# Optimization experiments

Measured on AMD Instinct MI355X. Metric: run time of the kernel, lower is better.

Reference implementation:

```python
import jax, jax.numpy as jnp
import numpy as np
from jax import lax

G, NPER, K = 64, 1024, 512          # graphs, nodes per graph, kept per graph (ceil(0.5*1024))
N, E = G * NPER, 1_048_576          # total nodes, total edges
F, H, C = 128, 128, 10              # in_feats, hidden_dim, num_classes


def gcn(x, src, dst, ew, W, b, num_nodes):
    """PyG GCNConv: D^{-1/2}(A+I)D^{-1/2} X W + b, with edge weights ew."""
    xw = x @ W                                              # [N, H]
    deg = jax.ops.segment_sum(ew, dst, num_segments=num_nodes) + 1.0  # +1 self loop
    dinv = lax.rsqrt(deg)
    coef = dinv[src] * dinv[dst] * ew                       # [E]
    agg = jax.ops.segment_sum(coef[:, None] * xw[src], dst, num_segments=num_nodes)
    return agg + (dinv * dinv)[:, None] * xw + b            # self-loop term + bias


def setup_inputs() -> dict:
    key = jax.random.key(0)
    ks = jax.random.split(key, 10)
    x = jax.random.normal(ks[0], (N, F), jnp.float32)
    # intra-graph random edges: dst forced into same graph block as src
    src = jax.random.randint(ks[1], (E,), 0, N, dtype=jnp.int32)
    dst = (src // NPER) * NPER + jax.random.randint(ks[2], (E,), 0, NPER, dtype=jnp.int32)
    edge_index = jnp.stack([src, dst])                      # [2, E]
    batch = jnp.repeat(jnp.arange(G, dtype=jnp.int32), NPER)
    W1 = jax.random.normal(ks[3], (F, H), jnp.float32) / np.sqrt(F)
    b1 = jnp.zeros((H,), jnp.float32)
    p = jax.random.normal(ks[4], (H,), jnp.float32) / np.sqrt(H)   # TopKPooling score vector
    W2 = jax.random.normal(ks[5], (H, H), jnp.float32) / np.sqrt(H)
    b2 = jnp.zeros((H,), jnp.float32)
    Wl = jax.random.normal(ks[6], (H, C), jnp.float32) / np.sqrt(H)
    bl = jnp.zeros((C,), jnp.float32)
    return dict(x=x, edge_index=edge_index, batch=batch, W1=W1, b1=b1, p=p, W2=W2, b2=b2, Wl=Wl, bl=bl)


def reference(x, edge_index, batch, W1, b1, p, W2, b2, Wl, bl):
    src, dst = edge_index[0], edge_index[1]
    ew1 = jnp.ones((E,), x.dtype)
    h = jax.nn.relu(gcn(x, src, dst, ew1, W1, b1, N))       # conv1 + relu

    # --- TopKPooling: score = tanh(x.p/||p||), keep top-K per graph, gate x by score ---
    score = jnp.tanh((h @ p) / jnp.linalg.norm(p))          # [N]
    vals, idx = lax.top_k(score.reshape(G, NPER), K)        # per-graph top-k, [G, K]
    perm = (idx + jnp.arange(G, dtype=idx.dtype)[:, None] * NPER).reshape(-1)  # global ids [G*K]
    h2 = h[perm] * vals.reshape(-1, 1)                      # gated kept nodes [G*K, H]

    # edge re-index: keep only edges with both endpoints surviving (mask via weight 0)
    new_id = jnp.full((N,), -1, jnp.int32).at[perm].set(jnp.arange(G * K, dtype=jnp.int32))
    s2, d2 = new_id[src], new_id[dst]
    mask = (s2 >= 0) & (d2 >= 0)
    ew2 = mask.astype(h.dtype)
    s2 = jnp.where(mask, s2, 0)
    d2 = jnp.where(mask, d2, 0)

    h3 = jax.nn.relu(gcn(h2, s2, d2, ew2, W2, b2, G * K))   # conv2 + relu

    pooled = h3.reshape(G, K, H).mean(axis=1)               # global_mean_pool (equal counts)
    return pooled @ Wl + bl                                 # [G, C]
```

## Files before the change

### kernel.cpp

```cpp
#include <hip/hip_runtime.h>

#define NNODES 65536
#define NEDGES 1048576
#define NGRAPH 64
#define NPERG  1024
#define KEEP   512
#define M2     (NGRAPH * KEEP)
#define HD     128
#define NC     10
#define EMAX   20480

#define OW1 0
#define OW2 16384
#define OWL 32768
#define OB1 34048
#define OB2 34176
#define OP  34304
#define OBL 34432
#define NCVT 34448

typedef __attribute__((ext_vector_type(8))) short bf16x8;
typedef __attribute__((ext_vector_type(4))) float f32x4;

__device__ __forceinline__ float bf2f(unsigned short u) {
    return __uint_as_float(((unsigned int)u) << 16);
}
__device__ __forceinline__ unsigned short f2bf(float f) {
    unsigned int u = __float_as_uint(f);
    unsigned int r = (u + 0x7FFFu + ((u >> 16) & 1u)) >> 16;
    return (unsigned short)r;
}

__global__ __launch_bounds__(256) void prep_kernel(
    const void* __restrict__ W1, const void* __restrict__ b1, const void* __restrict__ p,
    const void* __restrict__ W2, const void* __restrict__ b2, const void* __restrict__ Wl,
    const void* __restrict__ bl, int* __restrict__ flag, float* __restrict__ cw,
    float* __restrict__ invnorm, int* __restrict__ new_id, int* __restrict__ ghist,
    int* __restrict__ gcur0, float* __restrict__ pooled,
    unsigned short* __restrict__ w1t, unsigned short* __restrict__ w2t,
    const int* __restrict__ src, int* __restrict__ phist) {
    int bid = blockIdx.x, t = threadIdx.x;
    const unsigned short* w1u = (const unsigned short*)W1;
    int local = 0;
    for (int i = t; i < 512; i += 256) {
        unsigned short u = w1u[2 * i];
        int e = (u >> 7) & 0xFF;
        local += (e >= 100 && e <= 140) ? 1 : 0;
    }
    __shared__ int red[256];
    __shared__ int lh[NGRAPH];
    red[t] = local;
    __syncthreads();
    for (int off = 128; off; off >>= 1) {
        if (t < off) red[t] += red[t + off];
        __syncthreads();
    }
    int fl = (red[0] >= 384) ? 1 : 0;
    if (bid == 0 && t == 0) flag[0] = fl;

    if (bid < 135) {
        int gid = bid * 256 + t;
        if (gid < NCVT) {
            const void* srcp; int idx;
            if (gid < OB1) {
                if (gid < OW2)      { srcp = W1; idx = gid - OW1; }
                else if (gid < OWL) { srcp = W2; idx = gid - OW2; }
                else                { srcp = Wl; idx = gid - OWL; }
            } else {
                if (gid < OB2)      { srcp = b1; idx = gid - OB1; }
                else if (gid < OP)  { srcp = b2; idx = gid - OB2; }
                else if (gid < OBL) { srcp = p;  idx = gid - OP; }
                else                { srcp = bl; idx = gid - OBL; }
            }
            float v;
            if (gid >= OWL && gid < OB1 && idx >= 1280) v = 0.f;
            else if (gid >= OBL && idx >= NC) v = 0.f;
            else if (fl) v = bf2f(((const unsigned short*)srcp)[idx]);
            else v = ((const float*)srcp)[idx];
            cw[gid] = v;
            if (gid < OW2) {
                int k = gid >> 7, n = gid & 127;
                w1t[n * 128 + k] = f2bf(v);
            } else if (gid < OWL) {
                int r = gid - OW2;
                int k = r >> 7, n = r & 127;
                w2t[n * 128 + k] = f2bf(v);
            }
        }
    } else if (bid == 135) {
        __shared__ float s2a[128];
        float pv = 0.f;
        if (t < 128) pv = fl ? bf2f(((const unsigned short*)p)[t]) : ((const float*)p)[t];
        if (t < 128) s2a[t] = pv * pv;
        __syncthreads();
        for (int off = 64; off; off >>= 1) {
            if (t < off) s2a[t] += s2a[t + off];
            __syncthreads();
        }
        if (t == 0) invnorm[0] = 1.0f / sqrtf(s2a[0]);
    } else if (bid < 392) {
        int i = (bid - 136) * 256 + t;
        new_id[i] = -1;
        if (i < NGRAPH) { ghist[i] = 0; gcur0[i] = 0; }
        if (i < NGRAPH * HD) pooled[i] = 0.f;
    } else {
        if (t < NGRAPH) lh[t] = 0;
        __syncthreads();
        int e0 = (bid - 392) * 4096;
        for (int k = 0; k < 16; k++) atomicAdd(&lh[src[e0 + k * 256 + t] >> 10], 1);
        __syncthreads();
        if (t < NGRAPH) phist[(bid - 392) * 64 + t] = lh[t];
    }
}

__global__ __launch_bounds__(256) void binpass_kernel(const int* __restrict__ src,
                                                      const int* __restrict__ dst,
                                                      const int* __restrict__ phist,
                                                      int* __restrict__ ghist,
                                                      int* __restrict__ gcur0,
                                                      unsigned int* __restrict__ elist) {
    __shared__ int gh[NGRAPH];
    __shared__ int gbS[NGRAPH];
    __shared__ int lh[NGRAPH];
    __shared__ int lbase[NGRAPH];
    __shared__ int qsum[4][NGRAPH];
    int tid = threadIdx.x;
    {
        int g = tid & 63, q = tid >> 6;
        int s = 0;
        for (int b = q * 64; b < q * 64 + 64; b++) s += phist[b * 64 + g];
        qsum[q][g] = s;
    }
    __syncthreads();
    if (tid < NGRAPH) {
        gh[tid] = qsum[0][tid] + qsum[1][tid] + qsum[2][tid] + qsum[3][tid];
        lh[tid] = 0;
        if (blockIdx.x == 0) ghist[tid] = gh[tid];
    }
    __syncthreads();
    if (tid == 0) {
        int s = 0;
        for (int i = 0; i < NGRAPH; i++) { gbS[i] = s; s += gh[i]; }
    }
    __syncthreads();
    int e0 = blockIdx.x * 4096;
    int gs[16]; unsigned int pk[16];
    for (int k = 0; k < 16; k++) {
        int e = e0 + k * 256 + tid;
        int s = src[e], d = dst[e];
        gs[k] = s >> 10;
        pk[k] = (unsigned)(s & 1023) | ((unsigned)(d & 1023) << 10);
        atomicAdd(&lh[gs[k]], 1);
    }
    __syncthreads();
    if (tid < NGRAPH) { lbase[tid] = gbS[tid] + atomicAdd(&gcur0[tid], lh[tid]); lh[tid] = 0; }
    __syncthreads();
    for (int k = 0; k < 16; k++) {
        int g = gs[k];
        int pos = lbase[g] + atomicAdd(&lh[g], 1);
        elist[pos] = pk[k];
    }
}

__global__ __launch_bounds__(1024) void g1csr_kernel(
    const unsigned int* __restrict__ elist, const int* __restrict__ ghist,
    unsigned short* __restrict__ csr16, int* __restrict__ node_base,
    int* __restrict__ deg_out, float* __restrict__ dinv_out,
    const void* __restrict__ Araw, const unsigned short* __restrict__ Wtb,
    unsigned int* __restrict__ Cb, const int* __restrict__ flag) {
    __shared__ unsigned short sc[EMAX];
    __shared__ int cnt[NPERG];
    __shared__ int cur[NPERG];
    __shared__ int wsum[16];
    __shared__ int gh[NGRAPH];
    __shared__ int baseS, nS;
    int bid = blockIdx.x, t = threadIdx.x;
    if (bid < NGRAPH) {
        int g = bid;
        cnt[t] = 0;
        if (t < NGRAPH) gh[t] = ghist[t];
        __syncthreads();
        if (t == 0) {
            int s = 0;
            for (int i = 0; i < g; i++) s += gh[i];
            baseS = s; nS = gh[g];
        }
        __syncthreads();
        int base = baseS;
        int n = nS; if (n > EMAX) n = EMAX;
        for (int j = t; j < n; j += 1024) atomicAdd(&cnt[(elist[base + j] >> 10) & 1023], 1);
        __syncthreads();
        int v = cnt[t];
        int lane = t & 63;
        int x = v;
        for (int off = 1; off < 64; off <<= 1) {
            int y = __shfl_up(x, off);
            if (lane >= off) x += y;
        }
        if (lane == 63) wsum[t >> 6] = x;
        __syncthreads();
        if (t < 16) {
            int wv = wsum[t];
            int wx = wv;
            for (int off = 1; off < 16; off <<= 1) {
                int y = __shfl_up(wx, off);
                if (t >= off) wx += y;
            }
            wsum[t] = wx - wv;
        }
        __syncthreads();
        int excl = x - v + wsum[t >> 6];
        cur[t] = excl;
        deg_out[g * NPERG + t] = v;
        dinv_out[g * NPERG + t] = rsqrtf((float)v + 1.0f);
        node_base[g * NPERG + t] = base + excl;
        __syncthreads();
        for (int j = t; j < n; j += 1024) {
            unsigned int pk = elist[base + j];
            int d = (pk >> 10) & 1023;
            int pos = atomicAdd(&cur[d], 1);
            sc[pos] = (unsigned short)(pk & 1023);
        }
        __syncthreads();
        for (int j = t; j < n; j += 1024) csr16[base + j] = sc[j];
        return;
    }
    int row0 = (bid - NGRAPH) * 256;
    int wave = t >> 6, lane = t & 63;
    int r0 = row0 + wave * 16;
    int row = r0 + (lane & 15);
    int ko = (lane >> 4) * 8;
    f32x4 acc[8];
#pragma unroll
    for (int c = 0; c < 8; c++) acc[c] = (f32x4){0.f, 0.f, 0.f, 0.f};
    bf16x8 afr[4];
    if (flag[0]) {
        const unsigned short* arow = (const unsigned short*)Araw + (size_t)row * HD + ko;
#pragma unroll
        for (int kk = 0; kk < 4; kk++) afr[kk] = *(const bf16x8*)(arow + kk * 32);
    } else {
        const float* arow = (const float*)Araw + (size_t)row * HD + ko;
#pragma unroll
        for (int kk = 0; kk < 4; kk++) {
            float4 f0 = *(const float4*)(arow + kk * 32);
            float4 f1 = *(const float4*)(arow + kk * 32 + 4);
            bf16x8 a;
            a[0] = (short)f2bf(f0.x); a[1] = (short)f2bf(f0.y);
            a[2] = (short)f2bf(f0.z); a[3] = (short)f2bf(f0.w);
            a[4] = (short)f2bf(f1.x); a[5] = (short)f2bf(f1.y);
            a[6] = (short)f2bf(f1.z); a[7] = (short)f2bf(f1.w);
            afr[kk] = a;
        }
    }
    const unsigned short* brow = Wtb + (lane & 15) * HD + ko;
#pragma unroll
    for (int kk = 0; kk < 4; kk++) {
#pragma unroll
        for (int c = 0; c < 8; c++) {
            bf16x8 b = *(const bf16x8*)(brow + c * 16 * HD + kk * 32);
            acc[c] = __builtin_amdgcn_mfma_f32_16x16x32_bf16(afr[kk], b, acc[c], 0, 0, 0);
        }
    }
    int orow0 = r0 + (lane >> 4) * 4;
    bool even = !(lane & 1);
#pragma unroll
    for (int c = 0; c < 8; c++) {
#pragma unroll
        for (int j = 0; j < 4; j++) {
            float v = acc[c][j];
            float pt = __shfl_xor(v, 1);
            if (even) {
                unsigned int u = (unsigned int)f2bf(v) | ((unsigned int)f2bf(pt) << 16);
                Cb[(size_t)(orow0 + j) * 64 + ((c * 16 + (lane & 15)) >> 1)] = u;
            }
        }
    }
}

__global__ __launch_bounds__(256) void s1_pull(const unsigned short* __restrict__ csr16,
                                               const int* __restrict__ node_base,
                                               const int* __restrict__ deg,
                                               const float* __restrict__ dinv,
                                               const unsigned int* __restrict__ xwb,
                                               const float* __restrict__ b1,
                                               const float* __restrict__ pvec,
                                               const float* __restrict__ invnorm,
                                               unsigned int* __restrict__ hb,
                                               float* __restrict__ score) {
    int b = blockIdx.x;
    int xcd = b & 7, j = b >> 3;
    int g = (j >> 8) * 8 + xcd;
    int n = g * NPERG + (j & 255) * 4 + (threadIdx.x >> 6);
    int lane = threadIdx.x & 63;
    int gb = g * NPERG;
    int base = node_base[n], cnt = deg[n];
    int e = 0; float ds = 0.f;
    if (lane < cnt) {
        e = csr16[base + lane];
        ds = dinv[gb + e];
    }
    float a0 = 0.f, a1 = 0.f;
    int klim = cnt < 64 ? cnt : 64;
    int k = 0;
    for (; k + 7 < klim; k += 8) {
        int s0 = __shfl(e, k),     s1 = __shfl(e, k + 1);
        int s2 = __shfl(e, k + 2), s3 = __shfl(e, k + 3);
        int s4 = __shfl(e, k + 4), s5 = __shfl(e, k + 5);
        int s6 = __shfl(e, k + 6), s7 = __shfl(e, k + 7);
        float d0 = __shfl(ds, k),     d1 = __shfl(ds, k + 1);
        float d2 = __shfl(ds, k + 2), d3 = __shfl(ds, k + 3);
        float d4 = __shfl(ds, k + 4), d5 = __shfl(ds, k + 5);
        float d6 = __shfl(ds, k + 6), d7 = __shfl(ds, k + 7);
        unsigned int u0 = xwb[(size_t)(gb + s0) * 64 + lane];
        unsigned int u1 = xwb[(size_t)(gb + s1) * 64 + lane];
        unsigned int u2 = xwb[(size_t)(gb + s2) * 64 + lane];
        unsigned int u3 = xwb[(size_t)(gb + s3) * 64 + lane];
        unsigned int u4 = xwb[(size_t)(gb + s4) * 64 + lane];
        unsigned int u5 = xwb[(size_t)(gb + s5) * 64 + lane];
        unsigned int u6 = xwb[(size_t)(gb + s6) * 64 + lane];
        unsigned int u7 = xwb[(size_t)(gb + s7) * 64 + lane];
        a0 += d0 * __uint_as_float(u0 << 16); a1 += d0 * __uint_as_float(u0 & 0xFFFF0000u);
        a0 += d1 * __uint_as_float(u1 << 16); a1 += d1 * __uint_as_float(u1 & 0xFFFF0000u);
        a0 += d2 * __uint_as_float(u2 << 16); a1 += d2 * __uint_as_float(u2 & 0xFFFF0000u);
        a0 += d3 * __uint_as_float(u3 << 16); a1 += d3 * __uint_as_float(u3 & 0xFFFF0000u);
        a0 += d4 * __uint_as_float(u4 << 16); a1 += d4 * __uint_as_float(u4 & 0xFFFF0000u);
        a0 += d5 * __uint_as_float(u5 << 16); a1 += d5 * __uint_as_float(u5 & 0xFFFF0000u);
        a0 += d6 * __uint_as_float(u6 << 16); a1 += d6 * __uint_as_float(u6 & 0xFFFF0000u);
        a0 += d7 * __uint_as_float(u7 << 16); a1 += d7 * __uint_as_float(u7 & 0xFFFF0000u);
    }
    for (; k + 3 < klim; k += 4) {
        int s0 = __shfl(e, k), s1 = __shfl(e, k + 1);
        int s2 = __shfl(e, k + 2), s3 = __shfl(e, k + 3);
        float d0 = __shfl(ds, k), d1 = __shfl(ds, k + 1);
        float d2 = __shfl(ds, k + 2), d3 = __shfl(ds, k + 3);
        unsigned int u0 = xwb[(size_t)(gb + s0) * 64 + lane];
        unsigned int u1 = xwb[(size_t)(gb + s1) * 64 + lane];
        unsigned int u2 = xwb[(size_t)(gb + s2) * 64 + lane];
        unsigned int u3 = xwb[(size_t)(gb + s3) * 64 + lane];
        a0 += d0 * __uint_as_float(u0 << 16); a1 += d0 * __uint_as_float(u0 & 0xFFFF0000u);
        a0 += d1 * __uint_as_float(u1 << 16); a1 += d1 * __uint_as_float(u1 & 0xFFFF0000u);
        a0 += d2 * __uint_as_float(u2 << 16); a1 += d2 * __uint_as_float(u2 & 0xFFFF0000u);
        a0 += d3 * __uint_as_float(u3 << 16); a1 += d3 * __uint_as_float(u3 & 0xFFFF0000u);
    }
    for (; k < klim; k++) {
        int sk = __shfl(e, k);
        float dk = __shfl(ds, k);
        unsigned int u = xwb[(size_t)(gb + sk) * 64 + lane];
        a0 += dk * __uint_as_float(u << 16); a1 += dk * __uint_as_float(u & 0xFFFF0000u);
    }
    for (; k < cnt; k++) {
        int sk = csr16[base + k];
        float dk = dinv[gb + sk];
        unsigned int u = xwb[(size_t)(gb + sk) * 64 + lane];
        a0 += dk * __uint_as_float(u << 16); a1 += dk * __uint_as_float(u & 0xFFFF0000u);
    }
    float dn = dinv[n];
    float self = dn * dn;
    unsigned int us = xwb[(size_t)n * 64 + lane];
    float2 bb = ((const float2*)b1)[lane];
    float h0 = fmaxf(dn * a0 + self * __uint_as_float(us << 16) + bb.x, 0.f);
    float h1 = fmaxf(dn * a1 + self * __uint_as_float(us & 0xFFFF0000u) + bb.y, 0.f);
    hb[(size_t)n * 64 + lane] = (unsigned int)f2bf(h0) | ((unsigned int)f2bf(h1) << 16);
    float2 pp = ((const float2*)pvec)[lane];
    float sv = h0 * pp.x + h1 * pp.y;
    for (int off = 32; off; off >>= 1) sv += __shfl_down(sv, off);
    if (lane == 0) score[n] = tanhf(sv * invnorm[0]);
}

__global__ __launch_bounds__(1024) void topk_kernel(const float* __restrict__ score,
                                                    float* __restrict__ vals,
                                                    int* __restrict__ perm,
                                                    int* __restrict__ new_id) {
    __shared__ float sv[1024];
    __shared__ int si[1024];
    int g = blockIdx.x, t = threadIdx.x;
    float v = score[g * NPERG + t];
    int idx = t;
    for (int k = 2; k <= 1024; k <<= 1) {
        for (int j = k >> 1; j > 0; j >>= 1) {
            bool desc = ((t & k) == 0);
            bool up = (t & j) != 0;
            float vb; int ib;
            if (j >= 64) {
                sv[t] = v; si[t] = idx;
                __syncthreads();
                vb = sv[t ^ j]; ib = si[t ^ j];
                bool cmp = (v > vb) || (v == vb && idx < ib);
                bool keep = up ? (cmp != desc) : (cmp == desc);
                if (!keep) { v = vb; idx = ib; }
                __syncthreads();
            } else {
                vb = __shfl_xor(v, j);
                ib = __shfl_xor(idx, j);
                bool cmp = (v > vb) || (v == vb && idx < ib);
                bool keep = up ? (cmp != desc) : (cmp == desc);
                if (!keep) { v = vb; idx = ib; }
            }
        }
    }
    if (t < KEEP) {
        int node = g * NPERG + idx;
        int slot = g * KEEP + t;
        vals[slot] = v;
        perm[slot] = node;
        new_id[node] = slot;
    }
}

__global__ __launch_bounds__(512) void g2deg_kernel(
    const unsigned int* __restrict__ elist, const int* __restrict__ ghist,
    const int* __restrict__ new_id, float* __restrict__ dinv2,
    const unsigned int* __restrict__ hb, const int* __restrict__ perm,
    const float* __restrict__ vals, const unsigned short* __restrict__ Wtb,
    unsigned int* __restrict__ Cb) {
    __shared__ int d2[KEEP];
    __shared__ int gh[NGRAPH];
    __shared__ int baseS, nS;
    int bid = blockIdx.x, t = threadIdx.x;
    if (bid < NGRAPH) {
        int g = bid;
        if (t < KEEP) d2[t] = 0;
        if (t < NGRAPH) gh[t] = ghist[t];
        __syncthreads();
        if (t == 0) {
            int s = 0;
            for (int i = 0; i < g; i++) s += gh[i];
            baseS = s; nS = gh[g];
        }
        __syncthreads();
        int base = baseS, n = nS;
        int gb = g * NPERG;
        int kb = g * KEEP;
        for (int j = t; j < n; j += 512) {
            unsigned int pk = elist[base + j];
            int s = pk & 1023, d = (pk >> 10) & 1023;
            int ns = new_id[gb + s], nd = new_id[gb + d];
            if (ns >= 0 && nd >= 0) atomicAdd(&d2[nd - kb], 1);
        }
        __syncthreads();
        if (t < KEEP) dinv2[kb + t] = rsqrtf((float)d2[t] + 1.0f);
        return;
    }
    int row0 = (bid - NGRAPH) * 128;
    int wave = t >> 6, lane = t & 63;
    int r0 = row0 + wave * 16;
    int m = r0 + (lane & 15);
    int ko = (lane >> 4) * 8;
    float sc = vals[m];
    const unsigned int* arow = hb + (size_t)perm[m] * 64 + (ko >> 1);
    bf16x8 afr[4];
#pragma unroll
    for (int kk = 0; kk < 4; kk++) {
        uint4 q = *(const uint4*)(arow + kk * 16);
        bf16x8 a;
        a[0] = (short)f2bf(bf2f((unsigned short)q.x) * sc);
        a[1] = (short)f2bf(bf2f((unsigned short)(q.x >> 16)) * sc);
        a[2] = (short)f2bf(bf2f((unsigned short)q.y) * sc);
        a[3] = (short)f2bf(bf2f((unsigned short)(q.y >> 16)) * sc);
        a[4] = (short)f2bf(bf2f((unsigned short)q.z) * sc);
        a[5] = (short)f2bf(bf2f((unsigned short)(q.z >> 16)) * sc);
        a[6] = (short)f2bf(bf2f((unsigned short)q.w) * sc);
        a[7] = (short)f2bf(bf2f((unsigned short)(q.w >> 16)) * sc);
        afr[kk] = a;
    }
    f32x4 acc[8];
#pragma unroll
    for (int c = 0; c < 8; c++) acc[c] = (f32x4){0.f, 0.f, 0.f, 0.f};
    const unsigned short* brow = Wtb + (lane & 15) * HD + ko;
#pragma unroll
    for (int kk = 0; kk < 4; kk++) {
#pragma unroll
        for (int c = 0; c < 8; c++) {
            bf16x8 b = *(const bf16x8*)(brow + c * 16 * HD + kk * 32);
            acc[c] = __builtin_amdgcn_mfma_f32_16x16x32_bf16(afr[kk], b, acc[c], 0, 0, 0);
        }
    }
    int orow0 = r0 + (lane >> 4) * 4;
    bool even = !(lane & 1);
#pragma unroll
    for (int c = 0; c < 8; c++) {
#pragma unroll
        for (int j = 0; j < 4; j++) {
            float v = acc[c][j];
            float pt = __shfl_xor(v, 1);
            if (even) {
                unsigned int u = (unsigned int)f2bf(v) | ((unsigned int)f2bf(pt) << 16);
                Cb[(size_t)(orow0 + j) * 64 + ((c * 16 + (lane & 15)) >> 1)] = u;
            }
        }
    }
}

__global__ __launch_bounds__(256) void s2_pull(const unsigned short* __restrict__ csr16,
                                               const int* __restrict__ node_base,
                                               const int* __restrict__ deg,
                                               const int* __restrict__ perm,
                                               const int* __restrict__ new_id,
                                               const float* __restrict__ dinv2,
                                               const unsigned int* __restrict__ xwb2,
                                               const float* __restrict__ b2,
                                               float* __restrict__ pooled) {
    __shared__ float pr[HD];
    __shared__ int cnk[4][64];
    __shared__ float cds[4][64];
    int tid = threadIdx.x;
    if (tid < HD) pr[tid] = 0.f;
    __syncthreads();
    int b = blockIdx.x;
    int xcd = b & 7, j = b >> 3;
    int g = (j >> 7) * 8 + xcd;
    int wv = tid >> 6;
    int m = g * KEEP + (j & 127) * 4 + wv;
    int lane = tid & 63;
    int node = perm[m];
    int gb = node & ~(NPERG - 1);
    int base = node_base[node], cnt = deg[node];
    int nk = 0; float ds = 0.f;
    if (lane < cnt) {
        int ns = new_id[gb + csr16[base + lane]];
        if (ns >= 0) { nk = ns; ds = dinv2[ns]; }
    }
    unsigned long long msk = __ballot(ds != 0.f);
    int pos = __popcll(msk & ((1ull << lane) - 1ull));
    if (ds != 0.f) { cnk[wv][pos] = nk; cds[wv][pos] = ds; }
    int na = __popcll(msk);
    float a0 = 0.f, a1 = 0.f;
    int k = 0;
    for (; k + 3 < na; k += 4) {
        int s0 = cnk[wv][k], s1 = cnk[wv][k + 1];
        int s2 = cnk[wv][k + 2], s3 = cnk[wv][k + 3];
        float d0 = cds[wv][k], d1 = cds[wv][k + 1];
        float d2 = cds[wv][k + 2], d3 = cds[wv][k + 3];
        unsigned int u0 = xwb2[(size_t)s0 * 64 + lane];
        unsigned int u1 = xwb2[(size_t)s1 * 64 + lane];
        unsigned int u2 = xwb2[(size_t)s2 * 64 + lane];
        unsigned int u3 = xwb2[(size_t)s3 * 64 + lane];
        a0 += d0 * __uint_as_float(u0 << 16); a1 += d0 * __uint_as_float(u0 & 0xFFFF0000u);
        a0 += d1 * __uint_as_float(u1 << 16); a1 += d1 * __uint_as_float(u1 & 0xFFFF0000u);
        a0 += d2 * __uint_as_float(u2 << 16); a1 += d2 * __uint_as_float(u2 & 0xFFFF0000u);
        a0 += d3 * __uint_as_float(u3 << 16); a1 += d3 * __uint_as_float(u3 & 0xFFFF0000u);
    }
    for (; k < na; k++) {
        int sk = cnk[wv][k];
        float dk = cds[wv][k];
        unsigned int u = xwb2[(size_t)sk * 64 + lane];
        a0 += dk * __uint_as_float(u << 16); a1 += dk * __uint_as_float(u & 0xFFFF0000u);
    }
    for (int kk = 64; kk < cnt; kk++) {
        int ns = new_id[gb + csr16[base + kk]];
        if (ns >= 0) {
            float dk = dinv2[ns];
            unsigned int u = xwb2[(size_t)ns * 64 + lane];
            a0 += dk * __uint_as_float(u << 16); a1 += dk * __uint_as_float(u & 0xFFFF0000u);
        }
    }
    float dn = dinv2[m];
    float self = dn * dn;
    unsigned int us = xwb2[(size_t)m * 64 + lane];
    float2 bb = ((const float2*)b2)[lane];
    float o0 = fmaxf(dn * a0 + self * __uint_as_float(us << 16) + bb.x, 0.f);
    float o1 = fmaxf(dn * a1 + self * __uint_as_float(us & 0xFFFF0000u) + bb.y, 0.f);
    atomicAdd(&pr[lane * 2], o0);
    atomicAdd(&pr[lane * 2 + 1], o1);
    __syncthreads();
    if (tid < HD) atomicAdd(&pooled[g * HD + tid], pr[tid]);
}

__global__ __launch_bounds__(128) void outk_kernel(const float* __restrict__ pooled,
                                                   const float* __restrict__ Wl,
                                                   const float* __restrict__ bl,
                                                   void* __restrict__ outv,
                                                   const int* __restrict__ flag) {
    int g = blockIdx.x, t = threadIdx.x;
    __shared__ float sp[HD];
    sp[t] = pooled[g * HD + t] * (1.0f / KEEP);
    __syncthreads();
    if (t < NC) {
        float acc = bl[t];
        for (int hh = 0; hh < HD; hh++) acc += sp[hh] * Wl[hh * NC + t];
        if (flag[0]) ((unsigned short*)outv)[g * NC + t] = f2bf(acc);
        else         ((float*)outv)[g * NC + t] = acc;
    }
}

extern "C" void kernel_launch(void* const* d_in, const int* in_sizes, int n_in,
                              void* d_out, int out_size, void* d_ws, size_t ws_size,
                              hipStream_t stream) {
    const int* ei   = (const int*)d_in[1];
    const int* srcv = ei;
    const int* dstv = ei + NEDGES;

    char* w = (char*)d_ws;
    const size_t MB = 1u << 20;
    const size_t KB = 1024;
    float* dinv1     = (float*)(w + 0);
    float* score     = (float*)(w + 256 * KB);
    float* vals      = (float*)(w + 512 * KB);
    int*   perm      = (int*)(w + 640 * KB);
    int*   new_id    = (int*)(w + 768 * KB);
    int*   deg1      = (int*)(w + 1024 * KB);
    int*   node_base = (int*)(w + 1280 * KB);
    float* dinv2     = (float*)(w + 1536 * KB);
    float* invnorm   = (float*)(w + 1664 * KB);
    int*   flag      = (int*)(w + 1664 * KB + 64);
    int*   ghist     = (int*)(w + 1664 * KB + 1024);
    int*   gcur0     = (int*)(w + 1664 * KB + 2048);
    float* cw        = (float*)(w + 1700 * KB);
    float* pooled    = (float*)(w + 1840 * KB);
    unsigned short* w1t = (unsigned short*)(w + 1880 * KB);
    unsigned short* w2t = (unsigned short*)(w + 1912 * KB);
    int* phist       = (int*)(w + 1944 * KB);
    unsigned int* xw1b = (unsigned int*)(w + 2 * MB);
    unsigned int* xw2b = (unsigned int*)(w + 18 * MB);
    unsigned int* hb = (unsigned int*)(w + 34 * MB);
    unsigned int* elist    = (unsigned int*)(w + 66 * MB);
    unsigned short* csr16  = (unsigned short*)(w + 70 * MB);

    float* W1f = cw + OW1; float* W2f = cw + OW2; float* Wlf = cw + OWL;
    float* b1f = cw + OB1; float* b2f = cw + OB2; float* pf  = cw + OP;
    float* blf = cw + OBL;
    (void)W1f; (void)W2f;

    prep_kernel<<<648, 256, 0, stream>>>(d_in[3], d_in[4], d_in[5], d_in[6], d_in[7],
                                         d_in[8], d_in[9], flag, cw, invnorm, new_id,
                                         ghist, gcur0, pooled, w1t, w2t, srcv, phist);
    binpass_kernel<<<256, 256, 0, stream>>>(srcv, dstv, phist, ghist, gcur0, elist);
    g1csr_kernel<<<NGRAPH + NNODES / 256, 1024, 0, stream>>>(
        elist, ghist, csr16, node_base, deg1, dinv1, d_in[0], w1t, xw1b, flag);
    s1_pull<<<NNODES / 4, 256, 0, stream>>>(csr16, node_base, deg1, dinv1, xw1b, b1f, pf,
                                            invnorm, hb, score);
    topk_kernel<<<NGRAPH, 1024, 0, stream>>>(score, vals, perm, new_id);
    g2deg_kernel<<<NGRAPH + M2 / 128, 512, 0, stream>>>(
        elist, ghist, new_id, dinv2, hb, perm, vals, w2t, xw2b);
    s2_pull<<<M2 / 4, 256, 0, stream>>>(csr16, node_base, deg1, perm, new_id, dinv2,
                                        xw2b, b2f, pooled);
    outk_kernel<<<NGRAPH, 128, 0, stream>>>(pooled, Wlf, blf, d_out, flag);

    (void)in_sizes; (void)n_in; (void)out_size; (void)ws_size;
}
```

Before: 255.7 us.

## Split per-graph CSR build into global degree atomics and parallel scatter kernel

Degree counting moves into the binning pass as global atomics, and the per-graph CSR construction is split. The g1 kernel now only scans degrees, and a new scatter kernel running 4 blocks per graph places edges with global atomic cursors. This replaces the 64 heavy 1024-thread blocks using 40KB of shared staging, which serialized the edge scatter per graph and limited occupancy. It also adds an 8-way unrolled gather loop in the second aggregation. The costs are one extra kernel launch, global atomics contention, and nondeterministic neighbor order within the CSR.

```diff
diff --git a/kernel.cpp b/kernel.cpp
--- a/kernel.cpp
+++ b/kernel.cpp
@@ -8,7 +8,6 @@
 #define M2     (NGRAPH * KEEP)
 #define HD     128
 #define NC     10
-#define EMAX   20480
 
 #define OW1 0
 #define OW2 16384
@@ -38,7 +37,8 @@
     float* __restrict__ invnorm, int* __restrict__ new_id, int* __restrict__ ghist,
     int* __restrict__ gcur0, float* __restrict__ pooled,
     unsigned short* __restrict__ w1t, unsigned short* __restrict__ w2t,
-    const int* __restrict__ src, int* __restrict__ phist) {
+    const int* __restrict__ src, int* __restrict__ phist,
+    int* __restrict__ deg1, int* __restrict__ cur) {
     int bid = blockIdx.x, t = threadIdx.x;
     const unsigned short* w1u = (const unsigned short*)W1;
     int local = 0;
@@ -101,6 +101,8 @@
     } else if (bid < 392) {
         int i = (bid - 136) * 256 + t;
         new_id[i] = -1;
+        deg1[i] = 0;
+        cur[i] = 0;
         if (i < NGRAPH) { ghist[i] = 0; gcur0[i] = 0; }
         if (i < NGRAPH * HD) pooled[i] = 0.f;
     } else {
@@ -118,7 +120,8 @@
                                                       const int* __restrict__ phist,
                                                       int* __restrict__ ghist,
                                                       int* __restrict__ gcur0,
-                                                      unsigned int* __restrict__ elist) {
+                                                      unsigned int* __restrict__ elist,
+                                                      int* __restrict__ deg1) {
     __shared__ int gh[NGRAPH];
     __shared__ int gbS[NGRAPH];
     __shared__ int lh[NGRAPH];
@@ -151,6 +154,7 @@
         gs[k] = s >> 10;
         pk[k] = (unsigned)(s & 1023) | ((unsigned)(d & 1023) << 10);
         atomicAdd(&lh[gs[k]], 1);
+        atomicAdd(&deg1[gs[k] * NPERG + (d & 1023)], 1);
     }
     __syncthreads();
     if (tid < NGRAPH) { lbase[tid] = gbS[tid] + atomicAdd(&gcur0[tid], lh[tid]); lh[tid] = 0; }
@@ -162,35 +166,26 @@
     }
 }
 
-__global__ __launch_bounds__(1024) void g1csr_kernel(
-    const unsigned int* __restrict__ elist, const int* __restrict__ ghist,
-    unsigned short* __restrict__ csr16, int* __restrict__ node_base,
-    int* __restrict__ deg_out, float* __restrict__ dinv_out,
+__global__ __launch_bounds__(1024) void g1scan_kernel(
+    const int* __restrict__ ghist, const int* __restrict__ deg1,
+    int* __restrict__ node_base, float* __restrict__ dinv_out,
     const void* __restrict__ Araw, const unsigned short* __restrict__ Wtb,
     unsigned int* __restrict__ Cb, const int* __restrict__ flag) {
-    __shared__ unsigned short sc[EMAX];
-    __shared__ int cnt[NPERG];
-    __shared__ int cur[NPERG];
     __shared__ int wsum[16];
     __shared__ int gh[NGRAPH];
-    __shared__ int baseS, nS;
+    __shared__ int baseS;
     int bid = blockIdx.x, t = threadIdx.x;
     if (bid < NGRAPH) {
         int g = bid;
-        cnt[t] = 0;
         if (t < NGRAPH) gh[t] = ghist[t];
         __syncthreads();
         if (t == 0) {
             int s = 0;
             for (int i = 0; i < g; i++) s += gh[i];
-            baseS = s; nS = gh[g];
-        }
-        __syncthreads();
-        int base = baseS;
-        int n = nS; if (n > EMAX) n = EMAX;
-        for (int j = t; j < n; j += 1024) atomicAdd(&cnt[(elist[base + j] >> 10) & 1023], 1);
-        __syncthreads();
-        int v = cnt[t];
+            baseS = s;
+        }
+        __syncthreads();
+        int v = deg1[g * NPERG + t];
         int lane = t & 63;
         int x = v;
         for (int off = 1; off < 64; off <<= 1) {
@@ -210,19 +205,8 @@
         }
         __syncthreads();
         int excl = x - v + wsum[t >> 6];
-        cur[t] = excl;
-        deg_out[g * NPERG + t] = v;
         dinv_out[g * NPERG + t] = rsqrtf((float)v + 1.0f);
-        node_base[g * NPERG + t] = base + excl;
-        __syncthreads();
-        for (int j = t; j < n; j += 1024) {
-            unsigned int pk = elist[base + j];
-            int d = (pk >> 10) & 1023;
-            int pos = atomicAdd(&cur[d], 1);
-            sc[pos] = (unsigned short)(pk & 1023);
-        }
-        __syncthreads();
-        for (int j = t; j < n; j += 1024) csr16[base + j] = sc[j];
+        node_base[g * NPERG + t] = baseS + excl;
         return;
     }
     int row0 = (bid - NGRAPH) * 256;
@@ -274,6 +258,36 @@
                 Cb[(size_t)(orow0 + j) * 64 + ((c * 16 + (lane & 15)) >> 1)] = u;
             }
         }
+    }
+}
+
+__global__ __launch_bounds__(256) void scatter_kernel(
+    const unsigned int* __restrict__ elist, const int* __restrict__ ghist,
+    const int* __restrict__ node_base, int* __restrict__ cur,
+    unsigned short* __restrict__ csr16) {
+    __shared__ int gh[NGRAPH];
+    __shared__ int baseS;
+    int b = blockIdx.x;
+    int g = b >> 2, q = b & 3;
+    int t = threadIdx.x;
+    if (t < NGRAPH) gh[t] = ghist[t];
+    __syncthreads();
+    if (t == 0) {
+        int s = 0;
+        for (int i = 0; i < g; i++) s += gh[i];
+        baseS = s;
+    }
+    __syncthreads();
+    int base = baseS, n = gh[g];
+    int chunk = (n + 3) >> 2;
+    int j0 = q * chunk;
+    int j1 = j0 + chunk; if (j1 > n) j1 = n;
+    int gb = g * NPERG;
+    for (int j = j0 + t; j < j1; j += 256) {
+        unsigned int pk = elist[base + j];
+        int d = (pk >> 10) & 1023;
+        int pos = node_base[gb + d] + atomicAdd(&cur[gb + d], 1);
+        csr16[pos] = (unsigned short)(pk & 1023);
     }
 }
 
@@ -526,6 +540,32 @@
     int na = __popcll(msk);
     float a0 = 0.f, a1 = 0.f;
     int k = 0;
+    for (; k + 7 < na; k += 8) {
+        int s0 = cnk[wv][k],     s1 = cnk[wv][k + 1];
+        int s2 = cnk[wv][k + 2], s3 = cnk[wv][k + 3];
+        int s4 = cnk[wv][k + 4], s5 = cnk[wv][k + 5];
+        int s6 = cnk[wv][k + 6], s7 = cnk[wv][k + 7];
+        float d0 = cds[wv][k],     d1 = cds[wv][k + 1];
+        float d2 = cds[wv][k + 2], d3 = cds[wv][k + 3];
+        float d4 = cds[wv][k + 4], d5 = cds[wv][k + 5];
+        float d6 = cds[wv][k + 6], d7 = cds[wv][k + 7];
+        unsigned int u0 = xwb2[(size_t)s0 * 64 + lane];
+        unsigned int u1 = xwb2[(size_t)s1 * 64 + lane];
+        unsigned int u2 = xwb2[(size_t)s2 * 64 + lane];
+        unsigned int u3 = xwb2[(size_t)s3 * 64 + lane];
+        unsigned int u4 = xwb2[(size_t)s4 * 64 + lane];
+        unsigned int u5 = xwb2[(size_t)s5 * 64 + lane];
+        unsigned int u6 = xwb2[(size_t)s6 * 64 + lane];
+        unsigned int u7 = xwb2[(size_t)s7 * 64 + lane];
+        a0 += d0 * __uint_as_float(u0 << 16); a1 += d0 * __uint_as_float(u0 & 0xFFFF0000u);
+        a0 += d1 * __uint_as_float(u1 << 16); a1 += d1 * __uint_as_float(u1 & 0xFFFF0000u);
+        a0 += d2 * __uint_as_float(u2 << 16); a1 += d2 * __uint_as_float(u2 & 0xFFFF0000u);
+        a0 += d3 * __uint_as_float(u3 << 16); a1 += d3 * __uint_as_float(u3 & 0xFFFF0000u);
+        a0 += d4 * __uint_as_float(u4 << 16); a1 += d4 * __uint_as_float(u4 & 0xFFFF0000u);
+        a0 += d5 * __uint_as_float(u5 << 16); a1 += d5 * __uint_as_float(u5 & 0xFFFF0000u);
+        a0 += d6 * __uint_as_float(u6 << 16); a1 += d6 * __uint_as_float(u6 & 0xFFFF0000u);
+        a0 += d7 * __uint_as_float(u7 << 16); a1 += d7 * __uint_as_float(u7 & 0xFFFF0000u);
+    }
     for (; k + 3 < na; k += 4) {
         int s0 = cnk[wv][k], s1 = cnk[wv][k + 1];
         int s2 = cnk[wv][k + 2], s3 = cnk[wv][k + 3];
@@ -613,6 +653,7 @@
     unsigned int* xw1b = (unsigned int*)(w + 2 * MB);
     unsigned int* xw2b = (unsigned int*)(w + 18 * MB);
     unsigned int* hb = (unsigned int*)(w + 34 * MB);
+    int* cur         = (int*)(w + 50 * MB);
     unsigned int* elist    = (unsigned int*)(w + 66 * MB);
     unsigned short* csr16  = (unsigned short*)(w + 70 * MB);
 
@@ -623,10 +664,12 @@
 
     prep_kernel<<<648, 256, 0, stream>>>(d_in[3], d_in[4], d_in[5], d_in[6], d_in[7],
                                          d_in[8], d_in[9], flag, cw, invnorm, new_id,
-                                         ghist, gcur0, pooled, w1t, w2t, srcv, phist);
-    binpass_kernel<<<256, 256, 0, stream>>>(srcv, dstv, phist, ghist, gcur0, elist);
-    g1csr_kernel<<<NGRAPH + NNODES / 256, 1024, 0, stream>>>(
-        elist, ghist, csr16, node_base, deg1, dinv1, d_in[0], w1t, xw1b, flag);
+                                         ghist, gcur0, pooled, w1t, w2t, srcv, phist,
+                                         deg1, cur);
+    binpass_kernel<<<256, 256, 0, stream>>>(srcv, dstv, phist, ghist, gcur0, elist, deg1);
+    g1scan_kernel<<<NGRAPH + NNODES / 256, 1024, 0, stream>>>(
+        ghist, deg1, node_base, dinv1, d_in[0], w1t, xw1b, flag);
+    scatter_kernel<<<NGRAPH * 4, 256, 0, stream>>>(elist, ghist, node_base, cur, csr16);
     s1_pull<<<NNODES / 4, 256, 0, stream>>>(csr16, node_base, deg1, dinv1, xw1b, b1f, pf,
                                             invnorm, hb, score);
     topk_kernel<<<NGRAPH, 1024, 0, stream>>>(score, vals, perm, new_id);
```

Result: slower. 316.3 us (+23.7%).
